# Kernel tuning notes

Hardware: AMD Instinct MI355X
Metric: run time of the kernel (lower is better)

The kernel has to match this reference:

```python
import jax, jax.numpy as jnp
import numpy as np

N, E = 50000, 800000
D = 64          # output_dim == d_s == d_e
H = 128         # psi hidden width
PSI_IN = 2 * D + 2 * D + D  # 320


def setup_inputs() -> dict:
    key = jax.random.key(0)
    ks = jax.random.split(key, 12)
    scale = lambda fan_in: 1.0 / np.sqrt(fan_in)
    return {
        "h_d_prev": jax.random.normal(ks[0], (N, D), jnp.float32),
        "h_s": jax.random.normal(ks[1], (N, D), jnp.float32),
        "edge_feat": jax.random.normal(ks[2], (E, D), jnp.float32),
        "sender": jax.random.randint(ks[3], (E,), 0, N, jnp.int32),
        "receiver": jax.random.randint(ks[4], (E,), 0, N, jnp.int32),
        # psi MLP params (all layers use relu, incl. last: final_activation=None)
        "W0": jax.random.normal(ks[5], (PSI_IN, H), jnp.float32) * scale(PSI_IN),
        "b0": jnp.zeros((H,), jnp.float32),
        "W1": jax.random.normal(ks[6], (H, H), jnp.float32) * scale(H),
        "b1": jnp.zeros((H,), jnp.float32),
        "W2": jax.random.normal(ks[7], (H, D), jnp.float32) * scale(H),
        "b2": jnp.zeros((D,), jnp.float32),
        # final linear transform W (no bias)
        "Wm": jax.random.normal(ks[8], (D, D), jnp.float32) * scale(D),
    }


def reference(h_d_prev, h_s, edge_feat, sender, receiver, W0, b0, W1, b1, W2, b2, Wm):
    # gather node feats to edges
    h_di = h_d_prev[sender]      # [E, D]
    h_dj = h_d_prev[receiver]    # [E, D]
    h_si = h_s[sender]           # [E, D]
    h_sj = h_s[receiver]         # [E, D]
    psi_in = jnp.concatenate([h_si, h_sj, h_di, h_dj, edge_feat], axis=-1)  # [E, 320]
    # psi MLP: relu on every layer (final_activation=None keeps default relu)
    x = jax.nn.relu(psi_in @ W0 + b0)
    x = jax.nn.relu(x @ W1 + b1)
    psi = jax.nn.relu(x @ W2 + b2)          # [E, D]
    s_ij = psi * (h_dj - h_di)              # [E, D]
    agg = jax.ops.segment_sum(s_ij, receiver, num_segments=h_d_prev.shape[0])  # [N, D]
    return h_d_prev + agg @ Wm
```

## Files before the change

kernel.cpp:

```cpp
#include <hip/hip_runtime.h>

#define NN   50000
#define EE   800000
#define DD   64
#define HH   128
#define KIN  320
#define TILE_E 64

typedef __bf16 bf16x8 __attribute__((ext_vector_type(8)));
typedef float  f32x4  __attribute__((ext_vector_type(4)));

#if __has_builtin(__builtin_amdgcn_cvt_pk_bf16_f32)
typedef __bf16 bf16x2_t __attribute__((ext_vector_type(2)));
__device__ __forceinline__ unsigned int pk2(float a, float b) {
  union { bf16x2_t v; unsigned int u; } cv;
  cv.v = __builtin_amdgcn_cvt_pk_bf16_f32(a, b);
  return cv.u;
}
__device__ __forceinline__ unsigned short f2bf(float a) {
  return (unsigned short)(pk2(a, a) & 0xFFFFu);
}
#else
__device__ __forceinline__ unsigned short f2bf(float f) {
  union { float f; unsigned int u; } v; v.f = f;
  unsigned int u = v.u + 0x7FFFu + ((v.u >> 16) & 1u);
  return (unsigned short)(u >> 16);
}
__device__ __forceinline__ unsigned int pk2(float a, float b) {
  return (unsigned int)f2bf(a) | ((unsigned int)f2bf(b) << 16);
}
#endif

__device__ __forceinline__ float bf2f(unsigned short b) {
  union { unsigned int u; float f; } v; v.u = ((unsigned int)b) << 16; return v.f;
}

__device__ __forceinline__ int psiIdx(int row, int kk) {
  return ((((row >> 4) * 10 + (kk >> 5)) << 6) + ((row & 15) << 2) + ((kk >> 3) & 3)) * 8
         + (kk & 7);
}

__global__ __launch_bounds__(256) void prep_weights(
    const float* __restrict__ W0,
    const float* __restrict__ W1,
    const float* __restrict__ W2,
    unsigned short* __restrict__ WT0,
    unsigned short* __restrict__ WT1,
    unsigned short* __restrict__ WT2) {
  int t = blockIdx.x * 256 + threadIdx.x;
  if (t < KIN * HH) {
    int k = t / HH, n = t % HH;
    WT0[n * KIN + k] = f2bf(W0[t]);
  } else if (t < KIN * HH + HH * HH) {
    int u = t - KIN * HH; int k = u / HH, n = u % HH;
    WT1[n * HH + k] = f2bf(W1[u]);
  } else {
    int u = t - KIN * HH - HH * HH; int k = u / DD, n = u % DD;
    WT2[n * HH + k] = f2bf(W2[u]);
  }
}

__global__ __launch_bounds__(256) void prep_tables(
    const float* __restrict__ hd, const float* __restrict__ hs,
    unsigned short* __restrict__ hdb, unsigned short* __restrict__ hsb) {
  int t = blockIdx.x * 256 + threadIdx.x;
  const int n = NN * DD / 8;
  const float* src; unsigned short* dst; int i;
  if (t < n) { src = hd; dst = hdb; i = t; }
  else       { src = hs; dst = hsb; i = t - n; }
  float4 a = *(const float4*)(src + (size_t)i * 8);
  float4 b = *(const float4*)(src + (size_t)i * 8 + 4);
  uint4 w;
  w.x = pk2(a.x, a.y); w.y = pk2(a.z, a.w);
  w.z = pk2(b.x, b.y); w.w = pk2(b.z, b.w);
  *(uint4*)(dst + (size_t)i * 8) = w;
}

__global__ __launch_bounds__(256, 4) void edge_mlp(
    const unsigned short* __restrict__ hdb,
    const unsigned short* __restrict__ hsb,
    const float* __restrict__ ef,
    const int* __restrict__ snd,
    const int* __restrict__ rcv,
    const unsigned short* __restrict__ WT0,
    const float* __restrict__ b0,
    const unsigned short* __restrict__ WT1,
    const float* __restrict__ b1,
    const unsigned short* __restrict__ WT2,
    const float* __restrict__ b2,
    float* __restrict__ agg)
{
  __shared__ __align__(16) unsigned short psi[TILE_E * KIN];

  const int tid  = threadIdx.x;
  const int e0   = blockIdx.x * TILE_E;
  const int wv   = tid >> 6;
  const int lane = tid & 63;
  const int ln   = lane & 15;
  const int quad = lane >> 4;

  int ridx[16];
  #pragma unroll
  for (int mt = 0; mt < 4; ++mt)
    #pragma unroll
    for (int i = 0; i < 4; ++i)
      ridx[mt * 4 + i] = rcv[e0 + mt * 16 + quad * 4 + i];

  #pragma unroll
  for (int i = 0; i < 10; ++i) {
    const int seg = i >> 1;
    int e = ((i << 5) + (tid >> 3)) & 63;
    int c = tid & 7;
    int unit = (((e >> 4) * 10 + seg * 2 + (c >> 2)) << 6) + ((e & 15) << 2) + (c & 3);
    uint4 w;
    if (seg < 4) {
      const unsigned short* tb = (seg & 2) ? hdb : hsb;
      const int* ix = (seg & 1) ? rcv : snd;
      w = *(const uint4*)(tb + (size_t)ix[e0 + e] * DD + c * 8);
    } else {
      const float* src = ef + (size_t)(e0 + e) * DD;
      float4 v0 = *(const float4*)(src + c * 8);
      float4 v1 = *(const float4*)(src + c * 8 + 4);
      w.x = pk2(v0.x, v0.y); w.y = pk2(v0.z, v0.w);
      w.z = pk2(v1.x, v1.y); w.w = pk2(v1.z, v1.w);
    }
    *(uint4*)(&psi[unit * 8]) = w;
  }
  __syncthreads();

  f32x4 acc0[4], acc1[4];

  {
    #pragma unroll
    for (int m = 0; m < 4; ++m) { acc0[m] = (f32x4){0,0,0,0}; acc1[m] = (f32x4){0,0,0,0}; }
    const unsigned short* wb0 = WT0 + (wv * 32 + ln) * KIN + quad * 8;
    const unsigned short* wb1 = wb0 + 16 * KIN;
    #pragma unroll
    for (int k0 = 0; k0 < 10; ++k0) {
      bf16x8 bf0 = *(const bf16x8*)(wb0 + k0 * 32);
      bf16x8 bf1 = *(const bf16x8*)(wb1 + k0 * 32);
      #pragma unroll
      for (int mt = 0; mt < 4; ++mt) {
        bf16x8 af = *(const bf16x8*)(&psi[(((mt * 10 + k0) << 6) + (ln << 2) + quad) * 8]);
        acc0[mt] = __builtin_amdgcn_mfma_f32_16x16x32_bf16(af, bf0, acc0[mt], 0, 0, 0);
        acc1[mt] = __builtin_amdgcn_mfma_f32_16x16x32_bf16(af, bf1, acc1[mt], 0, 0, 0);
      }
    }
  }
  __syncthreads();

  {
    float bv0 = b0[wv * 32 + ln];
    float bv1 = b0[wv * 32 + 16 + ln];
    #pragma unroll
    for (int mt = 0; mt < 4; ++mt) {
      #pragma unroll
      for (int i = 0; i < 4; ++i) {
        int base = ((mt * 10 + wv) << 6) + ((quad * 4 + i) << 2) + (ln >> 3);
        float v0 = acc0[mt][i] + bv0; v0 = v0 > 0.f ? v0 : 0.f;
        float v1 = acc1[mt][i] + bv1; v1 = v1 > 0.f ? v1 : 0.f;
        psi[base * 8 + (ln & 7)]       = f2bf(v0);
        psi[(base + 2) * 8 + (ln & 7)] = f2bf(v1);
      }
    }
  }
  __syncthreads();

  {
    #pragma unroll
    for (int m = 0; m < 4; ++m) { acc0[m] = (f32x4){0,0,0,0}; acc1[m] = (f32x4){0,0,0,0}; }
    const unsigned short* wb0 = WT1 + (wv * 32 + ln) * HH + quad * 8;
    const unsigned short* wb1 = wb0 + 16 * HH;
    #pragma unroll
    for (int k0 = 0; k0 < 4; ++k0) {
      bf16x8 bf0 = *(const bf16x8*)(wb0 + k0 * 32);
      bf16x8 bf1 = *(const bf16x8*)(wb1 + k0 * 32);
      #pragma unroll
      for (int mt = 0; mt < 4; ++mt) {
        bf16x8 af = *(const bf16x8*)(&psi[(((mt * 10 + k0) << 6) + (ln << 2) + quad) * 8]);
        acc0[mt] = __builtin_amdgcn_mfma_f32_16x16x32_bf16(af, bf0, acc0[mt], 0, 0, 0);
        acc1[mt] = __builtin_amdgcn_mfma_f32_16x16x32_bf16(af, bf1, acc1[mt], 0, 0, 0);
      }
    }
  }
  __syncthreads();

  {
    float bv0 = b1[wv * 32 + ln];
    float bv1 = b1[wv * 32 + 16 + ln];
    #pragma unroll
    for (int mt = 0; mt < 4; ++mt) {
      #pragma unroll
      for (int i = 0; i < 4; ++i) {
        int base = ((mt * 10 + wv) << 6) + ((quad * 4 + i) << 2) + (ln >> 3);
        float v0 = acc0[mt][i] + bv0; v0 = v0 > 0.f ? v0 : 0.f;
        float v1 = acc1[mt][i] + bv1; v1 = v1 > 0.f ? v1 : 0.f;
        psi[base * 8 + (ln & 7)]       = f2bf(v0);
        psi[(base + 2) * 8 + (ln & 7)] = f2bf(v1);
      }
    }
  }
  __syncthreads();

  {
    f32x4 acc[4];
    #pragma unroll
    for (int m = 0; m < 4; ++m) acc[m] = (f32x4){0,0,0,0};
    const unsigned short* wb = WT2 + (wv * 16 + ln) * HH + quad * 8;
    #pragma unroll
    for (int k0 = 0; k0 < 4; ++k0) {
      bf16x8 bf = *(const bf16x8*)(wb + k0 * 32);
      #pragma unroll
      for (int mt = 0; mt < 4; ++mt) {
        bf16x8 af = *(const bf16x8*)(&psi[(((mt * 10 + k0) << 6) + (ln << 2) + quad) * 8]);
        acc[mt] = __builtin_amdgcn_mfma_f32_16x16x32_bf16(af, bf, acc[mt], 0, 0, 0);
      }
    }
    int   col = wv * 16 + ln;
    float bv  = b2[col];
    #pragma unroll
    for (int mt = 0; mt < 4; ++mt) {
      #pragma unroll
      for (int i = 0; i < 4; ++i) {
        int row = mt * 16 + quad * 4 + i;
        float p  = acc[mt][i] + bv; p = p > 0.f ? p : 0.f;
        float di = bf2f(psi[psiIdx(row, 128 + col)]);
        float dj = bf2f(psi[psiIdx(row, 192 + col)]);
        float s  = p * (dj - di);
        atomicAdd(&agg[(size_t)ridx[mt * 4 + i] * DD + col], s);
      }
    }
  }
}

__global__ __launch_bounds__(256) void final_out(
    const float* __restrict__ hd,
    const float* __restrict__ agg,
    const float* __restrict__ Wm,
    float* __restrict__ out)
{
  __shared__ float wmf[DD * DD];
  __shared__ float arow[16 * 72];
  int tid = threadIdx.x;
  const float4* wm4 = (const float4*)Wm;
  float4* wf4 = (float4*)wmf;
  #pragma unroll
  for (int i = tid; i < DD * DD / 4; i += 256) wf4[i] = wm4[i];

  int r0 = blockIdx.x * 16;
  {
    float4 av = *(const float4*)(agg + (size_t)r0 * DD + tid * 4);
    int rr = tid >> 4, cc = (tid & 15) * 4;
    *(float4*)&arow[rr * 72 + cc] = av;
  }
  __syncthreads();

  int row = tid >> 4;
  int cq  = (tid & 15) * 4;
  f32x4 acc = (f32x4){0, 0, 0, 0};
  #pragma unroll
  for (int k = 0; k < DD; ++k) {
    float a = arow[row * 72 + k];
    f32x4 w = *(const f32x4*)&wmf[k * DD + cq];
    acc += a * w;
  }
  size_t o = ((size_t)(r0 + row)) * DD + cq;
  f32x4 h = *(const f32x4*)(hd + o);
  *(f32x4*)(out + o) = h + acc;
}

extern "C" void kernel_launch(void* const* d_in, const int* in_sizes, int n_in,
                              void* d_out, int out_size, void* d_ws, size_t ws_size,
                              hipStream_t stream) {
  const float* hd = (const float*)d_in[0];
  const float* hs = (const float*)d_in[1];
  const float* ef = (const float*)d_in[2];
  const int* snd  = (const int*)d_in[3];
  const int* rcv  = (const int*)d_in[4];
  const float* W0 = (const float*)d_in[5];
  const float* b0 = (const float*)d_in[6];
  const float* W1 = (const float*)d_in[7];
  const float* b1 = (const float*)d_in[8];
  const float* W2 = (const float*)d_in[9];
  const float* b2 = (const float*)d_in[10];
  const float* Wm = (const float*)d_in[11];
  float* out      = (float*)d_out;

  char* ws = (char*)d_ws;
  float* agg = (float*)ws;
  unsigned short* WT0 = (unsigned short*)(ws + 12800000);
  unsigned short* WT1 = WT0 + KIN * HH;
  unsigned short* WT2 = WT1 + HH * HH;
  unsigned short* hdb = WT2 + HH * DD;
  unsigned short* hsb = hdb + (size_t)NN * DD;
  hipMemsetAsync(agg, 0, (size_t)NN * DD * sizeof(float), stream);
  prep_weights<<<256, 256, 0, stream>>>(W0, W1, W2, WT0, WT1, WT2);
  prep_tables<<<NN * DD * 2 / 8 / 256, 256, 0, stream>>>(hd, hs, hdb, hsb);
  edge_mlp<<<EE / TILE_E, 256, 0, stream>>>(hdb, hsb, ef, snd, rcv,
                                            WT0, b0, WT1, b1, WT2, b2, agg);
  final_out<<<NN / 16, 256, 0, stream>>>(hd, agg, Wm, out);
}
```

Measured before the change: 536.8 us.

## Double edge_mlp block to 512 threads, splitting output columns across eight waves

The edge MLP block grows from 4 to 8 waves for the same 64-edge tile. In layers 0 and 1 each wave now computes 16 of the 128 output columns instead of 32. In the last layer the waves split the edge row-tiles, each taking two m-tiles with 16 columns. The gather loop shrinks to one pass of 5 segments per thread. This halves per-wave accumulator and register pressure and gives more waves per CU to hide gather and atomic latency, at the cost of more barrier participants and fewer MFMAs per weight fragment load.

Measured after the change: 592.7 us. 10.4% more time.

```diff
diff --git a/kernel.cpp b/kernel.cpp
--- a/kernel.cpp
+++ b/kernel.cpp
@@ -76,7 +76,7 @@
   *(uint4*)(dst + (size_t)i * 8) = w;
 }
 
-__global__ __launch_bounds__(256, 4) void edge_mlp(
+__global__ __launch_bounds__(512, 8) void edge_mlp(
     const unsigned short* __restrict__ hdb,
     const unsigned short* __restrict__ hsb,
     const float* __restrict__ ef,
@@ -98,117 +98,46 @@
   const int lane = tid & 63;
   const int ln   = lane & 15;
   const int quad = lane >> 4;
-
-  int ridx[16];
+  const int mtb  = (wv >> 2) * 2;
+
+  int ridx[8];
   #pragma unroll
-  for (int mt = 0; mt < 4; ++mt)
+  for (int t = 0; t < 2; ++t)
     #pragma unroll
     for (int i = 0; i < 4; ++i)
-      ridx[mt * 4 + i] = rcv[e0 + mt * 16 + quad * 4 + i];
-
-  #pragma unroll
-  for (int i = 0; i < 10; ++i) {
-    const int seg = i >> 1;
-    int e = ((i << 5) + (tid >> 3)) & 63;
-    int c = tid & 7;
-    int unit = (((e >> 4) * 10 + seg * 2 + (c >> 2)) << 6) + ((e & 15) << 2) + (c & 3);
-    uint4 w;
-    if (seg < 4) {
-      const unsigned short* tb = (seg & 2) ? hdb : hsb;
-      const int* ix = (seg & 1) ? rcv : snd;
-      w = *(const uint4*)(tb + (size_t)ix[e0 + e] * DD + c * 8);
-    } else {
-      const float* src = ef + (size_t)(e0 + e) * DD;
-      float4 v0 = *(const float4*)(src + c * 8);
-      float4 v1 = *(const float4*)(src + c * 8 + 4);
-      w.x = pk2(v0.x, v0.y); w.y = pk2(v0.z, v0.w);
-      w.z = pk2(v1.x, v1.y); w.w = pk2(v1.z, v1.w);
-    }
-    *(uint4*)(&psi[unit * 8]) = w;
-  }
-  __syncthreads();
-
-  f32x4 acc0[4], acc1[4];
-
-  {
-    #pragma unroll
-    for (int m = 0; m < 4; ++m) { acc0[m] = (f32x4){0,0,0,0}; acc1[m] = (f32x4){0,0,0,0}; }
-    const unsigned short* wb0 = WT0 + (wv * 32 + ln) * KIN + quad * 8;
-    const unsigned short* wb1 = wb0 + 16 * KIN;
+      ridx[t * 4 + i] = rcv[e0 + (mtb + t) * 16 + quad * 4 + i];
+
+  {
+    const int e = tid >> 3;
+    const int c = tid & 7;
+    #pragma unroll
+    for (int seg = 0; seg < 5; ++seg) {
+      int unit = (((e >> 4) * 10 + seg * 2 + (c >> 2)) << 6) + ((e & 15) << 2) + (c & 3);
+      uint4 w;
+      if (seg < 4) {
+        const unsigned short* tb = (seg & 2) ? hdb : hsb;
+        const int* ix = (seg & 1) ? rcv : snd;
+        w = *(const uint4*)(tb + (size_t)ix[e0 + e] * DD + c * 8);
+      } else {
+        const float* src = ef + (size_t)(e0 + e) * DD;
+        float4 v0 = *(const float4*)(src + c * 8);
+        float4 v1 = *(const float4*)(src + c * 8 + 4);
+        w.x = pk2(v0.x, v0.y); w.y = pk2(v0.z, v0.w);
+        w.z = pk2(v1.x, v1.y); w.w = pk2(v1.z, v1.w);
+      }
+      *(uint4*)(&psi[unit * 8]) = w;
+    }
+  }
+  __syncthreads();
+
+  f32x4 acc[4];
+
+  {
+    #pragma unroll
+    for (int m = 0; m < 4; ++m) acc[m] = (f32x4){0,0,0,0};
+    const unsigned short* wb = WT0 + (wv * 16 + ln) * KIN + quad * 8;
     #pragma unroll
     for (int k0 = 0; k0 < 10; ++k0) {
-      bf16x8 bf0 = *(const bf16x8*)(wb0 + k0 * 32);
-      bf16x8 bf1 = *(const bf16x8*)(wb1 + k0 * 32);
-      #pragma unroll
-      for (int mt = 0; mt < 4; ++mt) {
-        bf16x8 af = *(const bf16x8*)(&psi[(((mt * 10 + k0) << 6) + (ln << 2) + quad) * 8]);
-        acc0[mt] = __builtin_amdgcn_mfma_f32_16x16x32_bf16(af, bf0, acc0[mt], 0, 0, 0);
-        acc1[mt] = __builtin_amdgcn_mfma_f32_16x16x32_bf16(af, bf1, acc1[mt], 0, 0, 0);
-      }
-    }
-  }
-  __syncthreads();
-
-  {
-    float bv0 = b0[wv * 32 + ln];
-    float bv1 = b0[wv * 32 + 16 + ln];
-    #pragma unroll
-    for (int mt = 0; mt < 4; ++mt) {
-      #pragma unroll
-      for (int i = 0; i < 4; ++i) {
-        int base = ((mt * 10 + wv) << 6) + ((quad * 4 + i) << 2) + (ln >> 3);
-        float v0 = acc0[mt][i] + bv0; v0 = v0 > 0.f ? v0 : 0.f;
-        float v1 = acc1[mt][i] + bv1; v1 = v1 > 0.f ? v1 : 0.f;
-        psi[base * 8 + (ln & 7)]       = f2bf(v0);
-        psi[(base + 2) * 8 + (ln & 7)] = f2bf(v1);
-      }
-    }
-  }
-  __syncthreads();
-
-  {
-    #pragma unroll
-    for (int m = 0; m < 4; ++m) { acc0[m] = (f32x4){0,0,0,0}; acc1[m] = (f32x4){0,0,0,0}; }
-    const unsigned short* wb0 = WT1 + (wv * 32 + ln) * HH + quad * 8;
-    const unsigned short* wb1 = wb0 + 16 * HH;
-    #pragma unroll
-    for (int k0 = 0; k0 < 4; ++k0) {
-      bf16x8 bf0 = *(const bf16x8*)(wb0 + k0 * 32);
-      bf16x8 bf1 = *(const bf16x8*)(wb1 + k0 * 32);
-      #pragma unroll
-      for (int mt = 0; mt < 4; ++mt) {
-        bf16x8 af = *(const bf16x8*)(&psi[(((mt * 10 + k0) << 6) + (ln << 2) + quad) * 8]);
-        acc0[mt] = __builtin_amdgcn_mfma_f32_16x16x32_bf16(af, bf0, acc0[mt], 0, 0, 0);
-        acc1[mt] = __builtin_amdgcn_mfma_f32_16x16x32_bf16(af, bf1, acc1[mt], 0, 0, 0);
-      }
-    }
-  }
-  __syncthreads();
-
-  {
-    float bv0 = b1[wv * 32 + ln];
-    float bv1 = b1[wv * 32 + 16 + ln];
-    #pragma unroll
-    for (int mt = 0; mt < 4; ++mt) {
-      #pragma unroll
-      for (int i = 0; i < 4; ++i) {
-        int base = ((mt * 10 + wv) << 6) + ((quad * 4 + i) << 2) + (ln >> 3);
-        float v0 = acc0[mt][i] + bv0; v0 = v0 > 0.f ? v0 : 0.f;
-        float v1 = acc1[mt][i] + bv1; v1 = v1 > 0.f ? v1 : 0.f;
-        psi[base * 8 + (ln & 7)]       = f2bf(v0);
-        psi[(base + 2) * 8 + (ln & 7)] = f2bf(v1);
-      }
-    }
-  }
-  __syncthreads();
-
-  {
-    f32x4 acc[4];
-    #pragma unroll
-    for (int m = 0; m < 4; ++m) acc[m] = (f32x4){0,0,0,0};
-    const unsigned short* wb = WT2 + (wv * 16 + ln) * HH + quad * 8;
-    #pragma unroll
-    for (int k0 = 0; k0 < 4; ++k0) {
       bf16x8 bf = *(const bf16x8*)(wb + k0 * 32);
       #pragma unroll
       for (int mt = 0; mt < 4; ++mt) {
@@ -216,18 +145,81 @@
         acc[mt] = __builtin_amdgcn_mfma_f32_16x16x32_bf16(af, bf, acc[mt], 0, 0, 0);
       }
     }
-    int   col = wv * 16 + ln;
+  }
+  __syncthreads();
+
+  {
+    float bv = b0[wv * 16 + ln];
+    #pragma unroll
+    for (int mt = 0; mt < 4; ++mt) {
+      #pragma unroll
+      for (int i = 0; i < 4; ++i) {
+        int unit = ((mt * 10 + (wv >> 1)) << 6) + ((quad * 4 + i) << 2)
+                 + (wv & 1) * 2 + (ln >> 3);
+        float v = acc[mt][i] + bv; v = v > 0.f ? v : 0.f;
+        psi[unit * 8 + (ln & 7)] = f2bf(v);
+      }
+    }
+  }
+  __syncthreads();
+
+  {
+    #pragma unroll
+    for (int m = 0; m < 4; ++m) acc[m] = (f32x4){0,0,0,0};
+    const unsigned short* wb = WT1 + (wv * 16 + ln) * HH + quad * 8;
+    #pragma unroll
+    for (int k0 = 0; k0 < 4; ++k0) {
+      bf16x8 bf = *(const bf16x8*)(wb + k0 * 32);
+      #pragma unroll
+      for (int mt = 0; mt < 4; ++mt) {
+        bf16x8 af = *(const bf16x8*)(&psi[(((mt * 10 + k0) << 6) + (ln << 2) + quad) * 8]);
+        acc[mt] = __builtin_amdgcn_mfma_f32_16x16x32_bf16(af, bf, acc[mt], 0, 0, 0);
+      }
+    }
+  }
+  __syncthreads();
+
+  {
+    float bv = b1[wv * 16 + ln];
+    #pragma unroll
+    for (int mt = 0; mt < 4; ++mt) {
+      #pragma unroll
+      for (int i = 0; i < 4; ++i) {
+        int unit = ((mt * 10 + (wv >> 1)) << 6) + ((quad * 4 + i) << 2)
+                 + (wv & 1) * 2 + (ln >> 3);
+        float v = acc[mt][i] + bv; v = v > 0.f ? v : 0.f;
+        psi[unit * 8 + (ln & 7)] = f2bf(v);
+      }
+    }
+  }
+  __syncthreads();
+
+  {
+    f32x4 a2[2];
+    a2[0] = (f32x4){0,0,0,0}; a2[1] = (f32x4){0,0,0,0};
+    const unsigned short* wb = WT2 + ((wv & 3) * 16 + ln) * HH + quad * 8;
+    #pragma unroll
+    for (int k0 = 0; k0 < 4; ++k0) {
+      bf16x8 bf = *(const bf16x8*)(wb + k0 * 32);
+      #pragma unroll
+      for (int t = 0; t < 2; ++t) {
+        int mt = mtb + t;
+        bf16x8 af = *(const bf16x8*)(&psi[(((mt * 10 + k0) << 6) + (ln << 2) + quad) * 8]);
+        a2[t] = __builtin_amdgcn_mfma_f32_16x16x32_bf16(af, bf, a2[t], 0, 0, 0);
+      }
+    }
+    int   col = (wv & 3) * 16 + ln;
     float bv  = b2[col];
     #pragma unroll
-    for (int mt = 0; mt < 4; ++mt) {
+    for (int t = 0; t < 2; ++t) {
       #pragma unroll
       for (int i = 0; i < 4; ++i) {
-        int row = mt * 16 + quad * 4 + i;
-        float p  = acc[mt][i] + bv; p = p > 0.f ? p : 0.f;
+        int row = (mtb + t) * 16 + quad * 4 + i;
+        float p  = a2[t][i] + bv; p = p > 0.f ? p : 0.f;
         float di = bf2f(psi[psiIdx(row, 128 + col)]);
         float dj = bf2f(psi[psiIdx(row, 192 + col)]);
         float s  = p * (dj - di);
-        atomicAdd(&agg[(size_t)ridx[mt * 4 + i] * DD + col], s);
+        atomicAdd(&agg[(size_t)ridx[t * 4 + i] * DD + col], s);
       }
     }
   }
@@ -296,7 +288,7 @@
   hipMemsetAsync(agg, 0, (size_t)NN * DD * sizeof(float), stream);
   prep_weights<<<256, 256, 0, stream>>>(W0, W1, W2, WT0, WT1, WT2);
   prep_tables<<<NN * DD * 2 / 8 / 256, 256, 0, stream>>>(hd, hs, hdb, hsb);
-  edge_mlp<<<EE / TILE_E, 256, 0, stream>>>(hdb, hsb, ef, snd, rcv,
+  edge_mlp<<<EE / TILE_E, 512, 0, stream>>>(hdb, hsb, ef, snd, rcv,
                                             WT0, b0, WT1, b1, WT2, b2, agg);
   final_out<<<NN / 16, 256, 0, stream>>>(hd, agg, Wm, out);
 }
```
